# Kernel optimization log

Hardware: AMD Instinct MI355X
Metric: run time of the kernel (lower is better)

Reference implementation:

```python
import jax, jax.numpy as jnp
import numpy as np
from jax.ops import segment_sum

N_NODES = 50000


def graph_conv(src, dst, x, W, b, n_nodes):
    # DGL GraphConv with norm='both' (allow_zero_in_degree=True):
    # h = D_in^{-1/2} * A^T (D_out^{-1/2} * x) W + b, degrees clamped to >=1
    ones = jnp.ones(src.shape[0], dtype=x.dtype)
    deg_out = jnp.clip(segment_sum(ones, src, num_segments=n_nodes), 1.0)
    deg_in = jnp.clip(segment_sum(ones, dst, num_segments=n_nodes), 1.0)
    h = x * jax.lax.rsqrt(deg_out)[:, None]
    h = h @ W                      # apply weight before aggregation (mult_W first)
    m = segment_sum(h[src], dst, num_segments=n_nodes)  # sparse neighbor sum
    return m * jax.lax.rsqrt(deg_in)[:, None] + b


def setup_inputs() -> dict:
    key = jax.random.key(0)
    ks = jax.random.split(key, 10)
    n, e = N_NODES, 1600000
    d_in, h1, h2, h3 = 128, 128, 128, 64
    in_feat = jax.random.normal(ks[0], (n, d_in), dtype=jnp.float32)
    src = jax.random.randint(ks[1], (e,), 0, n, dtype=jnp.int32)
    dst = jax.random.randint(ks[2], (e,), 0, n, dtype=jnp.int32)
    s = lambda fi, fo: (1.0 / np.sqrt(fi)).astype(np.float32)
    W1 = jax.random.normal(ks[3], (d_in, h1), dtype=jnp.float32) * s(d_in, h1)
    b1 = jnp.zeros((h1,), dtype=jnp.float32)
    W2 = jax.random.normal(ks[4], (h1, h2), dtype=jnp.float32) * s(h1, h2)
    b2 = jnp.zeros((h2,), dtype=jnp.float32)
    Wf = jax.random.normal(ks[5], (h2, h3), dtype=jnp.float32) * s(h2, h3)
    bf = jnp.zeros((h3,), dtype=jnp.float32)
    return {"in_feat": in_feat, "src": src, "dst": dst,
            "W1": W1, "b1": b1, "W2": W2, "b2": b2, "Wf": Wf, "bf": bf}


def reference(in_feat, src, dst, W1, b1, W2, b2, Wf, bf):
    n = in_feat.shape[0]
    h = graph_conv(src, dst, in_feat, W1, b1, n)
    h = jax.nn.relu(h)
    # dropout(p=0.2) is identity in eval mode
    h = graph_conv(src, dst, h, W2, b2, n)
    return h @ Wf + bf
```

## Files before the change

kernel.cpp:

```cpp
#include <hip/hip_runtime.h>
#include <hip/hip_fp16.h>

#define FD 128
#define OD 64
#define RN 256
#define CHUNKS 256
#define NRMAX 1024

typedef _Float16 f16x8 __attribute__((ext_vector_type(8)));
typedef float    f32x4 __attribute__((ext_vector_type(4)));
typedef float    f32x2 __attribute__((ext_vector_type(2)));


__global__ __launch_bounds__(1024) void region_hist_kernel(const int* __restrict__ src,
                                                           const int* __restrict__ dst,
                                                           int* __restrict__ hist_g,
                                                           int* __restrict__ hist_gs,
                                                           int E, int NR, int CS) {
    __shared__ int hist[NRMAX];
    __shared__ int hist_s[NRMAX];
    int c = blockIdx.x;
    for (int t = threadIdx.x; t < NR; t += 1024) { hist[t] = 0; hist_s[t] = 0; }
    __syncthreads();
    int e0 = c * CS, e1 = min(e0 + CS, E);
    int nv = (e1 - e0) & ~3;
    for (int e = e0 + threadIdx.x * 4; e < e0 + nv; e += 4096) {
        int4 d = *(const int4*)(dst + e);
        int4 s = *(const int4*)(src + e);
        atomicAdd(&hist[d.x >> 8], 1);
        atomicAdd(&hist[d.y >> 8], 1);
        atomicAdd(&hist[d.z >> 8], 1);
        atomicAdd(&hist[d.w >> 8], 1);
        atomicAdd(&hist_s[s.x >> 8], 1);
        atomicAdd(&hist_s[s.y >> 8], 1);
        atomicAdd(&hist_s[s.z >> 8], 1);
        atomicAdd(&hist_s[s.w >> 8], 1);
    }
    for (int e = e0 + nv + threadIdx.x; e < e1; e += 1024) {
        atomicAdd(&hist[dst[e] >> 8], 1);
        atomicAdd(&hist_s[src[e] >> 8], 1);
    }
    __syncthreads();
    for (int t = threadIdx.x; t < NR; t += 1024) {
        hist_g[t * CHUNKS + c]  = hist[t];
        hist_gs[t * CHUNKS + c] = hist_s[t];
    }
}

__global__ __launch_bounds__(1024) void scanfold_kernel(const int* __restrict__ hist_g,
                                                        const int* __restrict__ hist_gs,
                                                        int* __restrict__ rstart,
                                                        int* __restrict__ cursor,
                                                        int* __restrict__ sstart,
                                                        int* __restrict__ scursor,
                                                        int NR, int E,
                                                        const float* __restrict__ W2,
                                                        const float* __restrict__ Wf,
                                                        const float* __restrict__ b2,
                                                        const float* __restrict__ bf,
                                                        const float* __restrict__ W1,
                                                        __half* __restrict__ W1t,
                                                        __half* __restrict__ Wct,
                                                        float* __restrict__ bc) {
    __shared__ int wsum[16];
    int tid = threadIdx.x, lane = tid & 63, w = tid >> 6;

    if (blockIdx.x >= 1) {
        int gid = (blockIdx.x - 1) * 1024 + tid;
        if (gid < FD * FD) {
            int col = gid >> 7, k = gid & 127;
            W1t[gid] = __float2half(W1[k * FD + col]);
        }
        if (gid < FD * OD) {
            int col = gid >> 7, k = gid & 127;
            float s = 0.f;
            for (int kk = 0; kk < FD; kk++) s += W2[k * FD + kk] * Wf[kk * OD + col];
            Wct[gid] = __float2half(s);
        }
        if (gid < OD) {
            float s = bf[gid];
            for (int k = 0; k < FD; k++) s += b2[k] * Wf[k * OD + gid];
            bc[gid] = s;
        }
        return;
    }

    int total = 0;
    if (tid < NR) {
        const int4* hp = (const int4*)(hist_g + (size_t)tid * CHUNKS);
        #pragma unroll 8
        for (int c4 = 0; c4 < CHUNKS / 4; c4++) {
            int4 h = hp[c4];
            total += h.x + h.y + h.z + h.w;
        }
    }
    int x = total;
    #pragma unroll
    for (int d = 1; d < 64; d <<= 1) {
        int t = __shfl_up(x, d, 64);
        if (lane >= d) x += t;
    }
    if (lane == 63) wsum[w] = x;
    __syncthreads();
    if (w == 0) {
        int s = (lane < 16) ? wsum[lane] : 0;
        #pragma unroll
        for (int d = 1; d < 16; d <<= 1) {
            int t = __shfl_up(s, d, 64);
            if (lane >= d) s += t;
        }
        if (lane < 16) wsum[lane] = s;
    }
    __syncthreads();
    int off = (w == 0) ? 0 : wsum[w - 1];
    if (tid < NR) {
        int start = x + off - total;
        rstart[tid] = start;
        int run = start;
        const int4* hp = (const int4*)(hist_g + (size_t)tid * CHUNKS);
        int4* cp = (int4*)(cursor + (size_t)tid * CHUNKS);
        #pragma unroll 8
        for (int c4 = 0; c4 < CHUNKS / 4; c4++) {
            int4 h = hp[c4];
            int4 o;
            o.x = run; run += h.x;
            o.y = run; run += h.y;
            o.z = run; run += h.z;
            o.w = run; run += h.w;
            cp[c4] = o;
        }
    }
    if (tid == 0) rstart[NR] = E;
    __syncthreads();
    total = 0;
    if (tid < NR) {
        const int4* hp = (const int4*)(hist_gs + (size_t)tid * CHUNKS);
        #pragma unroll 8
        for (int c4 = 0; c4 < CHUNKS / 4; c4++) {
            int4 h = hp[c4];
            total += h.x + h.y + h.z + h.w;
        }
    }
    x = total;
    #pragma unroll
    for (int d = 1; d < 64; d <<= 1) {
        int t = __shfl_up(x, d, 64);
        if (lane >= d) x += t;
    }
    if (lane == 63) wsum[w] = x;
    __syncthreads();
    if (w == 0) {
        int s = (lane < 16) ? wsum[lane] : 0;
        #pragma unroll
        for (int d = 1; d < 16; d <<= 1) {
            int t = __shfl_up(s, d, 64);
            if (lane >= d) s += t;
        }
        if (lane < 16) wsum[lane] = s;
    }
    __syncthreads();
    off = (w == 0) ? 0 : wsum[w - 1];
    if (tid < NR) {
        int start = x + off - total;
        sstart[tid] = start;
        int run = start;
        const int4* hp = (const int4*)(hist_gs + (size_t)tid * CHUNKS);
        int4* cp = (int4*)(scursor + (size_t)tid * CHUNKS);
        #pragma unroll 8
        for (int c4 = 0; c4 < CHUNKS / 4; c4++) {
            int4 h = hp[c4];
            int4 o;
            o.x = run; run += h.x;
            o.y = run; run += h.y;
            o.z = run; run += h.z;
            o.w = run; run += h.w;
            cp[c4] = o;
        }
    }
    if (tid == 0) sstart[NR] = E;
}

__global__ __launch_bounds__(1024) void partition_kernel(const int* __restrict__ src,
                                                         const int* __restrict__ dst,
                                                         const int* __restrict__ cursor,
                                                         const int* __restrict__ scursor,
                                                         int* __restrict__ epack,
                                                         unsigned char* __restrict__ spack,
                                                         int E, int NR, int CS) {
    __shared__ int cur[NRMAX];
    __shared__ int scur[NRMAX];
    int c = blockIdx.x;
    for (int t = threadIdx.x; t < NR; t += 1024) {
        cur[t]  = cursor[(size_t)t * CHUNKS + c];
        scur[t] = scursor[(size_t)t * CHUNKS + c];
    }
    __syncthreads();
    int e0 = c * CS, e1 = min(e0 + CS, E);
    int nv = (e1 - e0) & ~3;
    for (int e = e0 + threadIdx.x * 4; e < e0 + nv; e += 4096) {
        int4 d = *(const int4*)(dst + e);
        int4 s = *(const int4*)(src + e);
        int p0 = atomicAdd(&cur[d.x >> 8], 1);
        int p1 = atomicAdd(&cur[d.y >> 8], 1);
        int p2 = atomicAdd(&cur[d.z >> 8], 1);
        int p3 = atomicAdd(&cur[d.w >> 8], 1);
        epack[p0] = ((d.x & 255) << 17) | s.x;
        epack[p1] = ((d.y & 255) << 17) | s.y;
        epack[p2] = ((d.z & 255) << 17) | s.z;
        epack[p3] = ((d.w & 255) << 17) | s.w;
        int q0 = atomicAdd(&scur[s.x >> 8], 1);
        int q1 = atomicAdd(&scur[s.y >> 8], 1);
        int q2 = atomicAdd(&scur[s.z >> 8], 1);
        int q3 = atomicAdd(&scur[s.w >> 8], 1);
        spack[q0] = (unsigned char)(s.x & 255);
        spack[q1] = (unsigned char)(s.y & 255);
        spack[q2] = (unsigned char)(s.z & 255);
        spack[q3] = (unsigned char)(s.w & 255);
    }
    for (int e = e0 + nv + threadIdx.x; e < e1; e += 1024) {
        int d = dst[e], s = src[e];
        int pos = atomicAdd(&cur[d >> 8], 1);
        epack[pos] = ((d & 255) << 17) | s;
        int qos = atomicAdd(&scur[s >> 8], 1);
        spack[qos] = (unsigned char)(s & 255);
    }
}

__global__ __launch_bounds__(1024) void region_finish_kernel(const int* __restrict__ epack,
                                                             const int* __restrict__ rstart,
                                                             const unsigned char* __restrict__ spack,
                                                             const int* __restrict__ sstart,
                                                             const float* __restrict__ in_feat,
                                                             int* __restrict__ csrc,
                                                             int* __restrict__ row_start,
                                                             float* __restrict__ r_in,
                                                             float* __restrict__ r_out,
                                                             __half* __restrict__ Xs,
                                                             int N, int NR, int E) {
    __shared__ int cnt[RN];
    __shared__ int cur[RN];
    __shared__ int wsum[16];
    __shared__ float rloc[RN];
    const int r = blockIdx.x, tid = threadIdx.x;
    const int lane = tid & 63, w = tid >> 6;

    const int s0 = rstart[r], s1 = rstart[r + 1];
    if (tid < RN) cnt[tid] = 0;
    __syncthreads();
    for (int e = s0 + tid; e < s1; e += 1024)
        atomicAdd(&cnt[epack[e] >> 17], 1);
    __syncthreads();
    int cv = (tid < RN) ? cnt[tid] : 0;
    int x = cv;
    #pragma unroll
    for (int d = 1; d < 64; d <<= 1) {
        int t = __shfl_up(x, d, 64);
        if (lane >= d) x += t;
    }
    if (lane == 63 && w < 4) wsum[w] = x;
    __syncthreads();
    if (tid < RN) {
        int woff = 0;
        for (int i = 0; i < w; i++) woff += wsum[i];
        int start = s0 + x - cv + woff;
        cur[tid] = start;
        int node = r * RN + tid;
        if (node < N) {
            row_start[node] = start;
            r_in[node] = rsqrtf((float)max(cv, 1));
        }
    }
    if (r == NR - 1 && tid == 0) row_start[N] = E;
    __syncthreads();
    for (int e = s0 + tid; e < s1; e += 1024) {
        int pk = epack[e];
        int pos = atomicAdd(&cur[pk >> 17], 1);
        csrc[pos] = pk & 0x1FFFF;
    }
    __syncthreads();

    const int t0 = sstart[r], t1 = sstart[r + 1];
    if (tid < RN) cnt[tid] = 0;
    __syncthreads();
    for (int e = t0 + tid; e < t1; e += 1024)
        atomicAdd(&cnt[spack[e]], 1);
    __syncthreads();
    if (tid < RN) {
        float ro = rsqrtf((float)max(cnt[tid], 1));
        rloc[tid] = ro;
        int node = r * RN + tid;
        if (node < N) r_out[node] = ro;
    }
    __syncthreads();

    for (int idx = tid; idx < RN * 32; idx += 1024) {
        int nrow = idx >> 5;
        int node = r * RN + nrow;
        if (node >= N) break;
        int gi = node * 32 + (idx & 31);
        float ro = rloc[nrow];
        float4 t = ((const float4*)in_feat)[gi];
        ((__half2*)Xs)[2 * gi]     = __floats2half2_rn(t.x * ro, t.y * ro);
        ((__half2*)Xs)[2 * gi + 1] = __floats2half2_rn(t.z * ro, t.w * ro);
    }
}

__global__ __launch_bounds__(256) void fused1_kernel(const __half* __restrict__ Xs,
                                                     const float* __restrict__ r_in,
                                                     const float* __restrict__ r_out,
                                                     const int* __restrict__ rs,
                                                     const int* __restrict__ csrc,
                                                     const __half* __restrict__ W1t,
                                                     const float* __restrict__ b1,
                                                     const __half* __restrict__ Wct,
                                                     __half* __restrict__ tbuf,
                                                     int N) {
    const int tid = threadIdx.x;
    const int lane = tid & 63, w = tid >> 6;
    const int l15 = lane & 15, quad = lane >> 4;
    const int base = blockIdx.x * 16;
    __shared__ __half2  zt[16][68];
    __shared__ _Float16 yt[16][136];

    const int col2 = 16 * w + l15;
    f16x8 bf1[2][4];
    #pragma unroll
    for (int nt = 0; nt < 2; nt++) {
        int col = 32 * w + 16 * nt + l15;
        const f16x8* bp = (const f16x8*)((const _Float16*)W1t + (size_t)col * FD + quad * 8);
        #pragma unroll
        for (int kk = 0; kk < 4; kk++) bf1[nt][kk] = bp[kk * 4];
    }
    f16x8 bf2[4];
    {
        const f16x8* bp = (const f16x8*)((const _Float16*)Wct + (size_t)col2 * FD + quad * 8);
        #pragma unroll
        for (int kk = 0; kk < 4; kk++) bf2[kk] = bp[kk * 4];
    }

    for (int j = 0; j < 4; j++) {
        const int row = 4 * j + w;
        const int v = base + row;
        float ax = 0.f, ay = 0.f;
        if (v < N) {
            int s0 = __builtin_amdgcn_readfirstlane(rs[v]);
            int s1 = __builtin_amdgcn_readfirstlane(rs[v + 1]);
            const int deg = s1 - s0;
            const int nb = deg >> 4;
            int e = s0;
            if (nb) {
                int ia[16];
                #pragma unroll
                for (int u = 0; u < 16; u++) ia[u] = csrc[e + u];
                for (int b = 1; b < nb; b++) {
                    __half2 t[16];
                    #pragma unroll
                    for (int u = 0; u < 16; u++)
                        t[u] = ((const __half2*)(Xs + (size_t)ia[u] * FD))[lane];
                    int eb = e + (b << 4);
                    #pragma unroll
                    for (int u = 0; u < 16; u++) ia[u] = csrc[eb + u];
                    #pragma unroll
                    for (int u = 0; u < 16; u++) {
                        float2 f = __half22float2(t[u]);
                        ax += f.x; ay += f.y;
                    }
                }
                __half2 t[16];
                #pragma unroll
                for (int u = 0; u < 16; u++)
                    t[u] = ((const __half2*)(Xs + (size_t)ia[u] * FD))[lane];
                #pragma unroll
                for (int u = 0; u < 16; u++) {
                    float2 f = __half22float2(t[u]);
                    ax += f.x; ay += f.y;
                }
                e += nb << 4;
            }
            const int rem = s1 - e;
            if (rem) {
                const int last = s1 - 1;
                int ia[16];
                #pragma unroll
                for (int u = 0; u < 16; u++) ia[u] = csrc[min(e + u, last)];
                #pragma unroll
                for (int u = 0; u < 16; u++) {
                    unsigned raw = ((const unsigned*)(Xs + (size_t)ia[u] * FD))[lane];
                    raw = (u < rem) ? raw : 0u;
                    union { unsigned q; __half2 h; } tt; tt.q = raw;
                    float2 f = __half22float2(tt.h);
                    ax += f.x; ay += f.y;
                }
            }
            float ri = r_in[v];
            zt[row][lane] = __floats2half2_rn(ax * ri, ay * ri);
        } else {
            zt[row][lane] = __floats2half2_rn(0.f, 0.f);
        }
    }
    __syncthreads();

    {
        const _Float16* Arow = (const _Float16*)&zt[l15][0] + quad * 8;
        f16x8 afrag[4];
        #pragma unroll
        for (int kk = 0; kk < 4; kk++) afrag[kk] = *(const f16x8*)(Arow + kk * 32);
        f32x4 acc0 = {0.f, 0.f, 0.f, 0.f};
        f32x4 acc1 = {0.f, 0.f, 0.f, 0.f};
        #pragma unroll
        for (int kk = 0; kk < 4; kk++) {
            acc0 = __builtin_amdgcn_mfma_f32_16x16x32_f16(afrag[kk], bf1[0][kk], acc0, 0, 0, 0);
            acc1 = __builtin_amdgcn_mfma_f32_16x16x32_f16(afrag[kk], bf1[1][kk], acc1, 0, 0, 0);
        }
        int c0 = 32 * w + l15, c1 = c0 + 16;
        float bb0 = b1[c0], bb1 = b1[c1];
        #pragma unroll
        for (int r = 0; r < 4; r++) {
            int row = quad * 4 + r;
            int v = base + row;
            float rsc = (v < N) ? r_out[v] : 0.f;
            yt[row][c0] = (_Float16)(fmaxf(acc0[r] + bb0, 0.f) * rsc);
            yt[row][c1] = (_Float16)(fmaxf(acc1[r] + bb1, 0.f) * rsc);
        }
    }
    __syncthreads();

    {
        const _Float16* Arow = &yt[l15][0] + quad * 8;
        f16x8 afrag[4];
        #pragma unroll
        for (int kk = 0; kk < 4; kk++) afrag[kk] = *(const f16x8*)(Arow + kk * 32);
        f32x4 acc = {0.f, 0.f, 0.f, 0.f};
        #pragma unroll
        for (int kk = 0; kk < 4; kk++)
            acc = __builtin_amdgcn_mfma_f32_16x16x32_f16(afrag[kk], bf2[kk], acc, 0, 0, 0);
        #pragma unroll
        for (int r = 0; r < 4; r++) {
            int row = quad * 4 + r;
            int v = base + row;
            if (v < N)
                tbuf[(size_t)v * OD + col2] = __float2half(acc[r]);
        }
    }
}

__global__ __launch_bounds__(256) void agg64_kernel(const __half* __restrict__ T,
                                                    const float* __restrict__ r_in,
                                                    const int* __restrict__ rs,
                                                    const int* __restrict__ csrc,
                                                    const float* __restrict__ bc,
                                                    float* __restrict__ out, int N) {
    const int tid = threadIdx.x;
    const int lane = tid & 63, wv = tid >> 6;
    const int hf = lane >> 5, l32 = lane & 31;
    int v = blockIdx.x * 8 + wv * 2 + hf;
    if (v >= N) return;
    int s0 = rs[v], s1 = rs[v + 1];
    const int deg = s1 - s0;
    float ax = 0.f, ay = 0.f;
    const int nb = deg >> 3;
    int e = s0;
    if (nb) {
        int ia[8];
        #pragma unroll
        for (int u = 0; u < 8; u++) ia[u] = csrc[e + u];
        for (int b = 1; b < nb; b++) {
            __half2 t[8];
            #pragma unroll
            for (int u = 0; u < 8; u++)
                t[u] = ((const __half2*)(T + (size_t)ia[u] * OD))[l32];
            int eb = e + (b << 3);
            #pragma unroll
            for (int u = 0; u < 8; u++) ia[u] = csrc[eb + u];
            #pragma unroll
            for (int u = 0; u < 8; u++) {
                float2 f = __half22float2(t[u]);
                ax += f.x; ay += f.y;
            }
        }
        __half2 t[8];
        #pragma unroll
        for (int u = 0; u < 8; u++)
            t[u] = ((const __half2*)(T + (size_t)ia[u] * OD))[l32];
        #pragma unroll
        for (int u = 0; u < 8; u++) {
            float2 f = __half22float2(t[u]);
            ax += f.x; ay += f.y;
        }
        e += nb << 3;
    }
    const int rem = s1 - e;
    if (rem) {
        const int last = s1 - 1;
        int ia[8];
        #pragma unroll
        for (int u = 0; u < 8; u++) ia[u] = csrc[min(e + u, last)];
        #pragma unroll
        for (int u = 0; u < 8; u++) {
            unsigned raw = ((const unsigned*)(T + (size_t)ia[u] * OD))[l32];
            raw = (u < rem) ? raw : 0u;
            union { unsigned q; __half2 h; } tt; tt.q = raw;
            float2 f = __half22float2(tt.h);
            ax += f.x; ay += f.y;
        }
    }
    float ri = r_in[v];
    f32x2 o;
    o.x = ax * ri + bc[l32 * 2];
    o.y = ay * ri + bc[l32 * 2 + 1];
    __builtin_nontemporal_store(o, (f32x2*)(out + (size_t)v * OD) + l32);
}

extern "C" void kernel_launch(void* const* d_in, const int* in_sizes, int n_in,
                              void* d_out, int out_size, void* d_ws, size_t ws_size,
                              hipStream_t stream) {
    const float* in_feat = (const float*)d_in[0];
    const int*   src     = (const int*)d_in[1];
    const int*   dst     = (const int*)d_in[2];
    const float* W1      = (const float*)d_in[3];
    const float* b1      = (const float*)d_in[4];
    const float* W2      = (const float*)d_in[5];
    const float* b2      = (const float*)d_in[6];
    const float* Wf      = (const float*)d_in[7];
    const float* bf      = (const float*)d_in[8];
    float* out = (float*)d_out;

    const int N = in_sizes[0] / FD;
    const int E = in_sizes[1];
    const int NR = (N + RN - 1) / RN;
    const int CS = (((E + CHUNKS - 1) / CHUNKS) + 3) & ~3;

    char* ws = (char*)d_ws;
    size_t off = 0;
    auto alloc = [&](size_t bytes) -> void* {
        void* p = ws + off;
        off += (bytes + 255) / 256 * 256;
        return p;
    };
    unsigned char* spack = (unsigned char*)alloc((size_t)E);
    int*    epack   = (int*)alloc((size_t)E * 4);
    __half* tbuf    = (__half*)spack;
    float*  r_out   = (float*)alloc((size_t)N * 4);
    float*  r_in    = (float*)alloc((size_t)N * 4);
    int*    hist_g  = (int*)alloc((size_t)CHUNKS * NRMAX * 4);
    int*    hist_gs = (int*)alloc((size_t)CHUNKS * NRMAX * 4);
    int*    cursor  = (int*)alloc((size_t)CHUNKS * NRMAX * 4);
    int*    scursor = (int*)alloc((size_t)CHUNKS * NRMAX * 4);
    int*    rstart  = (int*)alloc((size_t)(NR + 1) * 4);
    int*    sstart  = (int*)alloc((size_t)(NR + 1) * 4);
    int*    csrc    = (int*)alloc((size_t)E * 4);
    int*    row_start = (int*)alloc((size_t)(N + 1) * 4);
    __half* Xs      = (__half*)alloc((size_t)N * FD * 2);
    __half* W1t     = (__half*)alloc((size_t)FD * FD * 2);
    __half* Wct     = (__half*)alloc((size_t)OD * FD * 2);
    float*  bc      = (float*)alloc((size_t)OD * 4);
    (void)ws_size; (void)n_in; (void)out_size;

    region_hist_kernel<<<CHUNKS, 1024, 0, stream>>>(src, dst, hist_g, hist_gs, E, NR, CS);
    scanfold_kernel<<<17, 1024, 0, stream>>>(hist_g, hist_gs, rstart, cursor, sstart, scursor,
                                             NR, E, W2, Wf, b2, bf, W1, W1t, Wct, bc);
    partition_kernel<<<CHUNKS, 1024, 0, stream>>>(src, dst, cursor, scursor, epack, spack, E, NR, CS);
    region_finish_kernel<<<NR, 1024, 0, stream>>>(epack, rstart, spack, sstart, in_feat,
                                                  csrc, row_start, r_in, r_out, Xs, N, NR, E);
    fused1_kernel<<<(N + 15) / 16, 256, 0, stream>>>(Xs, r_in, r_out, row_start, csrc,
                                                     W1t, b1, Wct, tbuf, N);
    agg64_kernel<<<(N + 7) / 8, 256, 0, stream>>>(tbuf, r_in, row_start, csrc, bc, out, N);
}
```

Measured before the change: 259.7 us.

## Use one wave per node in fused1 with 1024-thread blocks

Blocks of fused1 grow from 256 to 1024 threads, so each of the 16 waves gathers one destination node's neighbors instead of each wave looping over four nodes. The MFMA stages are redistributed so 8 waves compute the first GEMM and 4 waves the second, and weight fragments are loaded after the gather instead of being held in registers throughout. This aims to raise memory-level parallelism in the gather and cut register pressure. The cost is larger blocks, idle waves during the GEMM phases, and per-wave weight reloads.

```diff
diff --git a/kernel.cpp b/kernel.cpp
--- a/kernel.cpp
+++ b/kernel.cpp
@@ -305,16 +305,16 @@
     }
 }
 
-__global__ __launch_bounds__(256) void fused1_kernel(const __half* __restrict__ Xs,
-                                                     const float* __restrict__ r_in,
-                                                     const float* __restrict__ r_out,
-                                                     const int* __restrict__ rs,
-                                                     const int* __restrict__ csrc,
-                                                     const __half* __restrict__ W1t,
-                                                     const float* __restrict__ b1,
-                                                     const __half* __restrict__ Wct,
-                                                     __half* __restrict__ tbuf,
-                                                     int N) {
+__global__ __launch_bounds__(1024, 8) void fused1_kernel(const __half* __restrict__ Xs,
+                                                         const float* __restrict__ r_in,
+                                                         const float* __restrict__ r_out,
+                                                         const int* __restrict__ rs,
+                                                         const int* __restrict__ csrc,
+                                                         const __half* __restrict__ W1t,
+                                                         const float* __restrict__ b1,
+                                                         const __half* __restrict__ Wct,
+                                                         __half* __restrict__ tbuf,
+                                                         int N) {
     const int tid = threadIdx.x;
     const int lane = tid & 63, w = tid >> 6;
     const int l15 = lane & 15, quad = lane >> 4;
@@ -322,25 +322,8 @@
     __shared__ __half2  zt[16][68];
     __shared__ _Float16 yt[16][136];
 
-    const int col2 = 16 * w + l15;
-    f16x8 bf1[2][4];
-    #pragma unroll
-    for (int nt = 0; nt < 2; nt++) {
-        int col = 32 * w + 16 * nt + l15;
-        const f16x8* bp = (const f16x8*)((const _Float16*)W1t + (size_t)col * FD + quad * 8);
-        #pragma unroll
-        for (int kk = 0; kk < 4; kk++) bf1[nt][kk] = bp[kk * 4];
-    }
-    f16x8 bf2[4];
     {
-        const f16x8* bp = (const f16x8*)((const _Float16*)Wct + (size_t)col2 * FD + quad * 8);
-        #pragma unroll
-        for (int kk = 0; kk < 4; kk++) bf2[kk] = bp[kk * 4];
-    }
-
-    for (int j = 0; j < 4; j++) {
-        const int row = 4 * j + w;
-        const int v = base + row;
+        const int v = base + w;
         float ax = 0.f, ay = 0.f;
         if (v < N) {
             int s0 = __builtin_amdgcn_readfirstlane(rs[v]);
@@ -393,39 +376,44 @@
                 }
             }
             float ri = r_in[v];
-            zt[row][lane] = __floats2half2_rn(ax * ri, ay * ri);
+            zt[w][lane] = __floats2half2_rn(ax * ri, ay * ri);
         } else {
-            zt[row][lane] = __floats2half2_rn(0.f, 0.f);
-        }
-    }
-    __syncthreads();
-
-    {
+            zt[w][lane] = __floats2half2_rn(0.f, 0.f);
+        }
+    }
+    __syncthreads();
+
+    if (w < 8) {
+        const int col = 16 * w + l15;
+        const f16x8* bp = (const f16x8*)((const _Float16*)W1t + (size_t)col * FD + quad * 8);
+        f16x8 bf[4];
+        #pragma unroll
+        for (int kk = 0; kk < 4; kk++) bf[kk] = bp[kk * 4];
         const _Float16* Arow = (const _Float16*)&zt[l15][0] + quad * 8;
         f16x8 afrag[4];
         #pragma unroll
         for (int kk = 0; kk < 4; kk++) afrag[kk] = *(const f16x8*)(Arow + kk * 32);
-        f32x4 acc0 = {0.f, 0.f, 0.f, 0.f};
-        f32x4 acc1 = {0.f, 0.f, 0.f, 0.f};
-        #pragma unroll
-        for (int kk = 0; kk < 4; kk++) {
-            acc0 = __builtin_amdgcn_mfma_f32_16x16x32_f16(afrag[kk], bf1[0][kk], acc0, 0, 0, 0);
-            acc1 = __builtin_amdgcn_mfma_f32_16x16x32_f16(afrag[kk], bf1[1][kk], acc1, 0, 0, 0);
-        }
-        int c0 = 32 * w + l15, c1 = c0 + 16;
-        float bb0 = b1[c0], bb1 = b1[c1];
+        f32x4 acc = {0.f, 0.f, 0.f, 0.f};
+        #pragma unroll
+        for (int kk = 0; kk < 4; kk++)
+            acc = __builtin_amdgcn_mfma_f32_16x16x32_f16(afrag[kk], bf[kk], acc, 0, 0, 0);
+        float bb = b1[col];
         #pragma unroll
         for (int r = 0; r < 4; r++) {
             int row = quad * 4 + r;
             int v = base + row;
             float rsc = (v < N) ? r_out[v] : 0.f;
-            yt[row][c0] = (_Float16)(fmaxf(acc0[r] + bb0, 0.f) * rsc);
-            yt[row][c1] = (_Float16)(fmaxf(acc1[r] + bb1, 0.f) * rsc);
-        }
-    }
-    __syncthreads();
-
-    {
+            yt[row][col] = (_Float16)(fmaxf(acc[r] + bb, 0.f) * rsc);
+        }
+    }
+    __syncthreads();
+
+    if (w < 4) {
+        const int col = 16 * w + l15;
+        const f16x8* bp = (const f16x8*)((const _Float16*)Wct + (size_t)col * FD + quad * 8);
+        f16x8 bf[4];
+        #pragma unroll
+        for (int kk = 0; kk < 4; kk++) bf[kk] = bp[kk * 4];
         const _Float16* Arow = &yt[l15][0] + quad * 8;
         f16x8 afrag[4];
         #pragma unroll
@@ -433,13 +421,13 @@
         f32x4 acc = {0.f, 0.f, 0.f, 0.f};
         #pragma unroll
         for (int kk = 0; kk < 4; kk++)
-            acc = __builtin_amdgcn_mfma_f32_16x16x32_f16(afrag[kk], bf2[kk], acc, 0, 0, 0);
+            acc = __builtin_amdgcn_mfma_f32_16x16x32_f16(afrag[kk], bf[kk], acc, 0, 0, 0);
         #pragma unroll
         for (int r = 0; r < 4; r++) {
             int row = quad * 4 + r;
             int v = base + row;
             if (v < N)
-                tbuf[(size_t)v * OD + col2] = __float2half(acc[r]);
+                tbuf[(size_t)v * OD + col] = __float2half(acc[r]);
         }
     }
 }
@@ -562,7 +550,7 @@
     partition_kernel<<<CHUNKS, 1024, 0, stream>>>(src, dst, cursor, scursor, epack, spack, E, NR, CS);
     region_finish_kernel<<<NR, 1024, 0, stream>>>(epack, rstart, spack, sstart, in_feat,
                                                   csrc, row_start, r_in, r_out, Xs, N, NR, E);
-    fused1_kernel<<<(N + 15) / 16, 256, 0, stream>>>(Xs, r_in, r_out, row_start, csrc,
-                                                     W1t, b1, Wct, tbuf, N);
+    fused1_kernel<<<(N + 15) / 16, 1024, 0, stream>>>(Xs, r_in, r_out, row_start, csrc,
+                                                      W1t, b1, Wct, tbuf, N);
     agg64_kernel<<<(N + 7) / 8, 256, 0, stream>>>(tbuf, r_in, row_start, csrc, bc, out, N);
 }
```

Measured after the change: 257.5 us. Within noise of the previous version (-0.9%).
